# Kernel tuning notes

Measured on AMD Instinct MI355X. Metric: run time of the kernel, lower is better.

## Reference

```python
import jax, jax.numpy as jnp
import numpy as np

N = 131072          # number of input points
M = 512             # num_prototypes
D = 64              # feature_dim
GAMMA = 1.0


def setup_inputs() -> dict:
    key = jax.random.key(0)
    kx, kp = jax.random.split(key)
    x = jax.random.normal(kx, (N, D), dtype=jnp.float32)
    prototypes = jax.random.normal(kp, (M, D), dtype=jnp.float32)
    return {"x": x, "prototypes": prototypes}


def reference(x, prototypes):
    x_sq = jnp.sum(x * x, axis=-1, keepdims=True)            # [N, 1]
    p_sq = jnp.sum(prototypes * prototypes, axis=-1)         # [M]
    cross = jnp.einsum('nd,md->nm', x, prototypes)           # [N, M]
    dist2 = x_sq + p_sq[None, :] - 2.0 * cross               # [N, M]
    dist2 = jnp.maximum(dist2, 0.0)                          # guard tiny negatives
    return jnp.exp(-GAMMA * dist2)
```

## Files before the change

### kernel.cpp

```cpp
#include <hip/hip_runtime.h>


#define N_PTS 131072
#define M_PROT 512
#define D_DIM 64
#define BN 32

typedef __attribute__((ext_vector_type(8))) short short8;
typedef __attribute__((ext_vector_type(4))) float f32x4;

union FragU { uint u[4]; short8 s; };

__device__ inline void load_split(const float* p, short8& hi, short8& lo, float& nrm) {
  const float4 a = *reinterpret_cast<const float4*>(p);
  const float4 b = *reinterpret_cast<const float4*>(p + 4);
  const float f[8] = {a.x, a.y, a.z, a.w, b.x, b.y, b.z, b.w};
  FragU H, L;
#pragma unroll
  for (int i = 0; i < 4; ++i) {
    const uint u0 = __float_as_uint(f[2 * i]);
    const uint u1 = __float_as_uint(f[2 * i + 1]);
    H.u[i] = (u0 >> 16) | (u1 & 0xFFFF0000u);
    const float l0 = f[2 * i]     - __uint_as_float(u0 & 0xFFFF0000u);
    const float l1 = f[2 * i + 1] - __uint_as_float(u1 & 0xFFFF0000u);
    L.u[i] = (__float_as_uint(l0) >> 16) | (__float_as_uint(l1) & 0xFFFF0000u);
    nrm = fmaf(f[2 * i], f[2 * i], nrm);
    nrm = fmaf(f[2 * i + 1], f[2 * i + 1], nrm);
  }
  hi = H.s;
  lo = L.s;
}

__global__ __launch_bounds__(256, 2)
void rbf_mfma(const float* __restrict__ x,
              const float* __restrict__ prot,
              float* __restrict__ out) {
  __shared__ float T[BN * M_PROT];

  const int tid = threadIdx.x;
  const int lane = tid & 63;
  const int w = tid >> 6;
  const int n0 = blockIdx.x * BN;
  const int lr = lane & 15;
  const int kg = (lane >> 4) * 8;
  const int m0w = w * 128;

  f32x4 acc[8][2];
#pragma unroll
  for (int i = 0; i < 8; ++i)
#pragma unroll
    for (int j = 0; j < 2; ++j) acc[i][j] = (f32x4){0.f, 0.f, 0.f, 0.f};

  float ps_part[8] = {0.f, 0.f, 0.f, 0.f, 0.f, 0.f, 0.f, 0.f};
  float xs_part[2] = {0.f, 0.f};

#pragma unroll
  for (int h = 0; h < 2; ++h) {
    short8 XH[2], XL[2];
#pragma unroll
    for (int fj = 0; fj < 2; ++fj)
      load_split(x + (size_t)(n0 + fj * 16 + lr) * D_DIM + h * 32 + kg,
                 XH[fj], XL[fj], xs_part[fj]);
#pragma unroll
    for (int fi = 0; fi < 8; ++fi) {
      short8 ph, pl;
      load_split(prot + (size_t)(m0w + fi * 16 + lr) * D_DIM + h * 32 + kg,
                 ph, pl, ps_part[fi]);
#pragma unroll
      for (int fj = 0; fj < 2; ++fj) {
        acc[fi][fj] = __builtin_amdgcn_mfma_f32_16x16x32_bf16(ph, XH[fj], acc[fi][fj], 0, 0, 0);
        acc[fi][fj] = __builtin_amdgcn_mfma_f32_16x16x32_bf16(ph, XL[fj], acc[fi][fj], 0, 0, 0);
        acc[fi][fj] = __builtin_amdgcn_mfma_f32_16x16x32_bf16(pl, XH[fj], acc[fi][fj], 0, 0, 0);
      }
    }
  }

#pragma unroll
  for (int fi = 0; fi < 8; ++fi) {
    ps_part[fi] += __shfl_xor(ps_part[fi], 16);
    ps_part[fi] += __shfl_xor(ps_part[fi], 32);
  }
#pragma unroll
  for (int fj = 0; fj < 2; ++fj) {
    xs_part[fj] += __shfl_xor(xs_part[fj], 16);
    xs_part[fj] += __shfl_xor(xs_part[fj], 32);
  }
  const int src = (lane >> 4) * 4;

#pragma unroll
  for (int fi = 0; fi < 8; ++fi) {
    f32x4 psv;
#pragma unroll
    for (int r = 0; r < 4; ++r) psv[r] = __shfl(ps_part[fi], src + r);
#pragma unroll
    for (int fj = 0; fj < 2; ++fj) {
      const f32x4 c = acc[fi][fj];
      const float xsv = xs_part[fj];
      float4 e;
      e.x = __expf(fminf(fmaf(2.f, c[0], -xsv) - psv[0], 0.f));
      e.y = __expf(fminf(fmaf(2.f, c[1], -xsv) - psv[1], 0.f));
      e.z = __expf(fminf(fmaf(2.f, c[2], -xsv) - psv[2], 0.f));
      e.w = __expf(fminf(fmaf(2.f, c[3], -xsv) - psv[3], 0.f));
      const int n_rel = fj * 16 + lr;
      const int m = m0w + fi * 16 + src;
      const int byte = (n_rel * 2048 + m * 4) ^ ((n_rel & 7) << 4);
      *reinterpret_cast<float4*>(reinterpret_cast<char*>(T) + byte) = e;
    }
  }
  __syncthreads();

  const size_t outbase = (size_t)n0 * M_PROT;
#pragma unroll
  for (int i = 0; i < 16; ++i) {
    const int fidx = i * 1024 + tid * 4;
    const int n_rel = fidx >> 9;
    const int byte = (fidx * 4) ^ ((n_rel & 7) << 4);
    const float4 v = *reinterpret_cast<const float4*>(reinterpret_cast<const char*>(T) + byte);
    *reinterpret_cast<float4*>(out + outbase + fidx) = v;
  }
}

extern "C" void kernel_launch(void* const* d_in, const int* in_sizes, int n_in,
                              void* d_out, int out_size, void* d_ws, size_t ws_size,
                              hipStream_t stream) {
  const float* x = (const float*)d_in[0];
  const float* p = (const float*)d_in[1];
  float* out = (float*)d_out;
  (void)in_sizes; (void)n_in; (void)out_size; (void)d_ws; (void)ws_size;
  rbf_mfma<<<N_PTS / BN, 256, 0, stream>>>(x, p, out);
}
```

Before: 348.0 us.

## Precompute bf16 hi/lo splits and norms in prepass kernels, halve LDS staging

Adds two prepass kernels that split x and the prototypes into bf16 hi/lo halves and compute their squared norms into the workspace. The main kernel then loads the pre-split fragments directly instead of redoing the split for every block, which matters most for the prototypes since every block repeats that work. It also halves the LDS staging buffer by writing output in two 16-row passes, so occupancy can rise to 4 blocks per CU. The cost is extra launches and a full read plus write of x in bf16 pairs (32 MB written, then read back), and the old single kernel is kept as a fallback when the workspace is too small.

```diff
diff --git a/kernel.cpp b/kernel.cpp
--- a/kernel.cpp
+++ b/kernel.cpp
@@ -9,13 +9,138 @@
 typedef __attribute__((ext_vector_type(8))) short short8;
 typedef __attribute__((ext_vector_type(4))) float f32x4;
 
-union FragU { uint u[4]; short8 s; };
-
-__device__ inline void load_split(const float* p, short8& hi, short8& lo, float& nrm) {
+__global__ __launch_bounds__(256) void split_p(const float* __restrict__ p,
+                                               ushort* __restrict__ ph,
+                                               ushort* __restrict__ pl,
+                                               float* __restrict__ ps) {
+  const int row = blockIdx.x * 4 + (threadIdx.x >> 6);
+  const int d = threadIdx.x & 63;
+  const float v = p[row * D_DIM + d];
+  const uint u = __float_as_uint(v);
+  const float hf = __uint_as_float(u & 0xFFFF0000u);
+  ph[row * D_DIM + d] = (ushort)(u >> 16);
+  pl[row * D_DIM + d] = (ushort)(__float_as_uint(v - hf) >> 16);
+  float s = v * v;
+  s += __shfl_xor(s, 1);  s += __shfl_xor(s, 2);  s += __shfl_xor(s, 4);
+  s += __shfl_xor(s, 8);  s += __shfl_xor(s, 16); s += __shfl_xor(s, 32);
+  if (d == 0) ps[row] = s;
+}
+
+__global__ __launch_bounds__(256) void split_x(const float* __restrict__ x,
+                                               ushort* __restrict__ xh,
+                                               ushort* __restrict__ xl,
+                                               float* __restrict__ xs) {
+  const int gid = blockIdx.x * 256 + threadIdx.x;
+  const int row = gid >> 3;
+  const int c0 = (gid & 7) * 8;
+  const float4 a = *reinterpret_cast<const float4*>(x + (size_t)row * D_DIM + c0);
+  const float4 b = *reinterpret_cast<const float4*>(x + (size_t)row * D_DIM + c0 + 4);
+  const float f[8] = {a.x, a.y, a.z, a.w, b.x, b.y, b.z, b.w};
+  union { uint u[4]; short8 s; } H, L;
+  float part = 0.f;
+#pragma unroll
+  for (int i = 0; i < 4; ++i) {
+    const uint u0 = __float_as_uint(f[2 * i]);
+    const uint u1 = __float_as_uint(f[2 * i + 1]);
+    H.u[i] = (u0 >> 16) | (u1 & 0xFFFF0000u);
+    const float l0 = f[2 * i]     - __uint_as_float(u0 & 0xFFFF0000u);
+    const float l1 = f[2 * i + 1] - __uint_as_float(u1 & 0xFFFF0000u);
+    L.u[i] = (__float_as_uint(l0) >> 16) | (__float_as_uint(l1) & 0xFFFF0000u);
+    part = fmaf(f[2 * i], f[2 * i], part);
+    part = fmaf(f[2 * i + 1], f[2 * i + 1], part);
+  }
+  *reinterpret_cast<short8*>(xh + (size_t)row * D_DIM + c0) = H.s;
+  *reinterpret_cast<short8*>(xl + (size_t)row * D_DIM + c0) = L.s;
+  part += __shfl_xor(part, 1); part += __shfl_xor(part, 2); part += __shfl_xor(part, 4);
+  if ((threadIdx.x & 7) == 0) xs[row] = part;
+}
+
+__global__ __launch_bounds__(256, 4)
+void rbf_main(const ushort* __restrict__ xh, const ushort* __restrict__ xl,
+              const ushort* __restrict__ ph, const ushort* __restrict__ pl,
+              const float* __restrict__ xs, const float* __restrict__ ps,
+              float* __restrict__ out) {
+  __shared__ float T[16 * M_PROT];
+
+  const int tid = threadIdx.x;
+  const int lane = tid & 63;
+  const int w = tid >> 6;
+  const int n0 = blockIdx.x * BN;
+  const int lr = lane & 15;
+  const int kg = (lane >> 4) * 8;
+  const int m0w = w * 128;
+  const int src = (lane >> 4) * 4;
+
+  short8 XH[2][2], XL[2][2];
+#pragma unroll
+  for (int h = 0; h < 2; ++h)
+#pragma unroll
+    for (int fj = 0; fj < 2; ++fj) {
+      const size_t off = (size_t)(n0 + fj * 16 + lr) * D_DIM + h * 32 + kg;
+      XH[h][fj] = *reinterpret_cast<const short8*>(xh + off);
+      XL[h][fj] = *reinterpret_cast<const short8*>(xl + off);
+    }
+
+  f32x4 acc[8][2];
+#pragma unroll
+  for (int i = 0; i < 8; ++i)
+#pragma unroll
+    for (int j = 0; j < 2; ++j) acc[i][j] = (f32x4){0.f, 0.f, 0.f, 0.f};
+
+#pragma unroll
+  for (int h = 0; h < 2; ++h)
+#pragma unroll
+    for (int fi = 0; fi < 8; ++fi) {
+      const size_t off = (size_t)(m0w + fi * 16 + lr) * D_DIM + h * 32 + kg;
+      const short8 a = *reinterpret_cast<const short8*>(ph + off);
+      const short8 b = *reinterpret_cast<const short8*>(pl + off);
+#pragma unroll
+      for (int fj = 0; fj < 2; ++fj) {
+        acc[fi][fj] = __builtin_amdgcn_mfma_f32_16x16x32_bf16(a, XH[h][fj], acc[fi][fj], 0, 0, 0);
+        acc[fi][fj] = __builtin_amdgcn_mfma_f32_16x16x32_bf16(a, XL[h][fj], acc[fi][fj], 0, 0, 0);
+        acc[fi][fj] = __builtin_amdgcn_mfma_f32_16x16x32_bf16(b, XH[h][fj], acc[fi][fj], 0, 0, 0);
+      }
+    }
+
+  const float xsv0 = xs[n0 + lr];
+  const float xsv1 = xs[n0 + 16 + lr];
+
+#pragma unroll
+  for (int fj = 0; fj < 2; ++fj) {
+    if (fj) __syncthreads();
+    const float xsv = fj ? xsv1 : xsv0;
+#pragma unroll
+    for (int fi = 0; fi < 8; ++fi) {
+      const int m = m0w + fi * 16 + src;
+      const f32x4 psv = *reinterpret_cast<const f32x4*>(ps + m);
+      const f32x4 c = acc[fi][fj];
+      float4 e;
+      e.x = __expf(fminf(fmaf(2.f, c[0], -xsv) - psv[0], 0.f));
+      e.y = __expf(fminf(fmaf(2.f, c[1], -xsv) - psv[1], 0.f));
+      e.z = __expf(fminf(fmaf(2.f, c[2], -xsv) - psv[2], 0.f));
+      e.w = __expf(fminf(fmaf(2.f, c[3], -xsv) - psv[3], 0.f));
+      const int byte = (lr * 2048 + m * 4) ^ ((lr & 7) << 4);
+      *reinterpret_cast<float4*>(reinterpret_cast<char*>(T) + byte) = e;
+    }
+    __syncthreads();
+    const size_t outbase = (size_t)(n0 + fj * 16) * M_PROT;
+#pragma unroll
+    for (int i = 0; i < 8; ++i) {
+      const int fidx = i * 1024 + tid * 4;
+      const int nloc = fidx >> 9;
+      const int byte = (fidx * 4) ^ ((nloc & 7) << 4);
+      const float4 v = *reinterpret_cast<const float4*>(reinterpret_cast<const char*>(T) + byte);
+      *reinterpret_cast<float4*>(out + outbase + fidx) = v;
+    }
+  }
+}
+
+union FragUF { uint u[4]; short8 s; };
+__device__ inline void load_splitF(const float* p, short8& hi, short8& lo, float& nrm) {
   const float4 a = *reinterpret_cast<const float4*>(p);
   const float4 b = *reinterpret_cast<const float4*>(p + 4);
   const float f[8] = {a.x, a.y, a.z, a.w, b.x, b.y, b.z, b.w};
-  FragU H, L;
+  FragUF H, L;
 #pragma unroll
   for (int i = 0; i < 4; ++i) {
     const uint u0 = __float_as_uint(f[2 * i]);
@@ -27,66 +152,47 @@
     nrm = fmaf(f[2 * i], f[2 * i], nrm);
     nrm = fmaf(f[2 * i + 1], f[2 * i + 1], nrm);
   }
-  hi = H.s;
-  lo = L.s;
-}
-
+  hi = H.s; lo = L.s;
+}
 __global__ __launch_bounds__(256, 2)
-void rbf_mfma(const float* __restrict__ x,
-              const float* __restrict__ prot,
-              float* __restrict__ out) {
+void rbf_fallback(const float* __restrict__ x, const float* __restrict__ prot,
+                  float* __restrict__ out) {
   __shared__ float T[BN * M_PROT];
-
-  const int tid = threadIdx.x;
-  const int lane = tid & 63;
-  const int w = tid >> 6;
-  const int n0 = blockIdx.x * BN;
-  const int lr = lane & 15;
-  const int kg = (lane >> 4) * 8;
-  const int m0w = w * 128;
-
+  const int tid = threadIdx.x, lane = tid & 63, w = tid >> 6;
+  const int n0 = blockIdx.x * BN, lr = lane & 15, kg = (lane >> 4) * 8, m0w = w * 128;
   f32x4 acc[8][2];
 #pragma unroll
   for (int i = 0; i < 8; ++i)
 #pragma unroll
     for (int j = 0; j < 2; ++j) acc[i][j] = (f32x4){0.f, 0.f, 0.f, 0.f};
-
-  float ps_part[8] = {0.f, 0.f, 0.f, 0.f, 0.f, 0.f, 0.f, 0.f};
-  float xs_part[2] = {0.f, 0.f};
-
+  float ps_part[8] = {0,0,0,0,0,0,0,0}, xs_part[2] = {0,0};
 #pragma unroll
   for (int h = 0; h < 2; ++h) {
-    short8 XH[2], XL[2];
+    short8 XHf[2], XLf[2];
 #pragma unroll
     for (int fj = 0; fj < 2; ++fj)
-      load_split(x + (size_t)(n0 + fj * 16 + lr) * D_DIM + h * 32 + kg,
-                 XH[fj], XL[fj], xs_part[fj]);
+      load_splitF(x + (size_t)(n0 + fj * 16 + lr) * D_DIM + h * 32 + kg, XHf[fj], XLf[fj], xs_part[fj]);
 #pragma unroll
     for (int fi = 0; fi < 8; ++fi) {
-      short8 ph, pl;
-      load_split(prot + (size_t)(m0w + fi * 16 + lr) * D_DIM + h * 32 + kg,
-                 ph, pl, ps_part[fi]);
+      short8 a, b;
+      load_splitF(prot + (size_t)(m0w + fi * 16 + lr) * D_DIM + h * 32 + kg, a, b, ps_part[fi]);
 #pragma unroll
       for (int fj = 0; fj < 2; ++fj) {
-        acc[fi][fj] = __builtin_amdgcn_mfma_f32_16x16x32_bf16(ph, XH[fj], acc[fi][fj], 0, 0, 0);
-        acc[fi][fj] = __builtin_amdgcn_mfma_f32_16x16x32_bf16(ph, XL[fj], acc[fi][fj], 0, 0, 0);
-        acc[fi][fj] = __builtin_amdgcn_mfma_f32_16x16x32_bf16(pl, XH[fj], acc[fi][fj], 0, 0, 0);
+        acc[fi][fj] = __builtin_amdgcn_mfma_f32_16x16x32_bf16(a, XHf[fj], acc[fi][fj], 0, 0, 0);
+        acc[fi][fj] = __builtin_amdgcn_mfma_f32_16x16x32_bf16(a, XLf[fj], acc[fi][fj], 0, 0, 0);
+        acc[fi][fj] = __builtin_amdgcn_mfma_f32_16x16x32_bf16(b, XHf[fj], acc[fi][fj], 0, 0, 0);
       }
     }
   }
-
 #pragma unroll
   for (int fi = 0; fi < 8; ++fi) {
-    ps_part[fi] += __shfl_xor(ps_part[fi], 16);
-    ps_part[fi] += __shfl_xor(ps_part[fi], 32);
+    ps_part[fi] += __shfl_xor(ps_part[fi], 16); ps_part[fi] += __shfl_xor(ps_part[fi], 32);
   }
 #pragma unroll
   for (int fj = 0; fj < 2; ++fj) {
-    xs_part[fj] += __shfl_xor(xs_part[fj], 16);
-    xs_part[fj] += __shfl_xor(xs_part[fj], 32);
+    xs_part[fj] += __shfl_xor(xs_part[fj], 16); xs_part[fj] += __shfl_xor(xs_part[fj], 32);
   }
   const int src = (lane >> 4) * 4;
-
 #pragma unroll
   for (int fi = 0; fi < 8; ++fi) {
     f32x4 psv;
@@ -108,7 +214,6 @@
     }
   }
   __syncthreads();
-
   const size_t outbase = (size_t)n0 * M_PROT;
 #pragma unroll
   for (int i = 0; i < 16; ++i) {
@@ -126,6 +231,29 @@
   const float* x = (const float*)d_in[0];
   const float* p = (const float*)d_in[1];
   float* out = (float*)d_out;
-  (void)in_sizes; (void)n_in; (void)out_size; (void)d_ws; (void)ws_size;
-  rbf_mfma<<<N_PTS / BN, 256, 0, stream>>>(x, p, out);
-}
+  (void)in_sizes; (void)n_in; (void)out_size;
+
+  const size_t xh_off = 0;
+  const size_t xl_off = xh_off + (size_t)N_PTS * D_DIM * 2;
+  const size_t ph_off = xl_off + (size_t)N_PTS * D_DIM * 2;
+  const size_t pl_off = ph_off + (size_t)M_PROT * D_DIM * 2;
+  const size_t ps_off = pl_off + (size_t)M_PROT * D_DIM * 2;
+  const size_t xs_off = ps_off + (size_t)M_PROT * 4;
+  const size_t need   = xs_off + (size_t)N_PTS * 4;
+
+  if (ws_size < need) {
+    rbf_fallback<<<N_PTS / BN, 256, 0, stream>>>(x, p, out);
+    return;
+  }
+  char* ws = (char*)d_ws;
+  ushort* xh = (ushort*)(ws + xh_off);
+  ushort* xl = (ushort*)(ws + xl_off);
+  ushort* ph = (ushort*)(ws + ph_off);
+  ushort* pl = (ushort*)(ws + pl_off);
+  float*  ps = (float*)(ws + ps_off);
+  float*  xs = (float*)(ws + xs_off);
+
+  split_p<<<M_PROT / 4, 256, 0, stream>>>(p, ph, pl, ps);
+  split_x<<<N_PTS * 8 / 256, 256, 0, stream>>>(x, xh, xl, xs);
+  rbf_main<<<N_PTS / BN, 256, 0, stream>>>(xh, xl, ph, pl, xs, ps, out);
+}
```

Result: slower. 356.7 us (+2.5%).
